# Kernel optimization log

Measured on AMD Instinct MI355X. Metric: run time of the kernel, lower is better.

The kernel has to match this reference:

```python
import jax, jax.numpy as jnp
import numpy as np

N_NODES = 100000
N_EDGES = 3200000
IN_FEATS = 512
HIDDEN = 16
NUM_CLASSES = 40


def setup_inputs() -> dict:
    key = jax.random.key(0)
    k1, k2, k3, k4, k5, k6 = jax.random.split(key, 6)
    x = jax.random.normal(k1, (N_NODES, IN_FEATS), dtype=jnp.float32)
    edge_index = jax.random.randint(k2, (2, N_EDGES), 0, N_NODES, dtype=jnp.int64)
    # Glorot-ish init for GCN weights
    W1 = jax.random.normal(k3, (IN_FEATS, HIDDEN), dtype=jnp.float32) / np.sqrt(IN_FEATS)
    b1 = jnp.zeros((HIDDEN,), dtype=jnp.float32)
    W2 = jax.random.normal(k4, (HIDDEN, NUM_CLASSES), dtype=jnp.float32) / np.sqrt(HIDDEN)
    b2 = jnp.zeros((NUM_CLASSES,), dtype=jnp.float32)
    return {"x": x, "edge_index": edge_index, "W1": W1, "b1": b1, "W2": W2, "b2": b2}


def _gcn_norm(edge_index, num_nodes):
    # Add self-loops (PyG GCNConv default), then symmetric normalization
    loops = jnp.arange(num_nodes, dtype=edge_index.dtype)
    src = jnp.concatenate([edge_index[0], loops])
    dst = jnp.concatenate([edge_index[1], loops])
    deg = jax.ops.segment_sum(jnp.ones_like(dst, dtype=jnp.float32), dst,
                              num_segments=num_nodes)
    dinv = jnp.where(deg > 0, jax.lax.rsqrt(deg), 0.0)
    norm = dinv[src] * dinv[dst]  # [E + N]
    return src, dst, norm


def _gcn_conv(x, W, b, src, dst, norm, num_nodes):
    h = x @ W                                   # transform first: [N, d_out]
    msg = h[src] * norm[:, None]                # gather + scale: [E+N, d_out]
    agg = jax.ops.segment_sum(msg, dst, num_segments=num_nodes)
    return agg + b


def reference(x, edge_index, W1, b1, W2, b2):
    num_nodes = x.shape[0]
    src, dst, norm = _gcn_norm(edge_index, num_nodes)
    h = _gcn_conv(x, W1, b1, src, dst, norm, num_nodes)
    h = jax.nn.relu(h)
    # F.dropout(training=self.training): eval mode -> identity (deterministic reference)
    h = _gcn_conv(h, W2, b2, src, dst, norm, num_nodes)
    return jax.nn.log_softmax(h, axis=1)
```

## Files before the change

### kernel.cpp

```cpp
#include <hip/hip_runtime.h>
#include <hip/hip_bf16.h>
#include <math.h>

#define N_NODES 100000
#define N_EDGES 3200000
#define IN_F    512
#define HID     16
#define NCLS    40
#define NB      2048
#define NPB     49
#define CAPW    2048
#define NBLK    256
#define EPB     12500
#define GEMM_BLKS 391

typedef unsigned short ushort_t;

__device__ __forceinline__ float bf16_to_f32(ushort_t u) {
    unsigned int b = ((unsigned int)u) << 16;
    return __uint_as_float(b);
}
__device__ __forceinline__ ushort_t f32_to_bf16(float f) {
    __hip_bfloat16 h = __float2bfloat16(f);
    return *(ushort_t*)&h;
}

__device__ __forceinline__ int load_edge(const void* ei, int is64, int idx) {
    if (is64) return (int)((const long long*)ei)[idx];
    return ((const int*)ei)[idx];
}

__global__ __launch_bounds__(256) void kPre(const int* __restrict__ ei,
                                            int* __restrict__ flag,
                                            int* __restrict__ gcur) {
    int i = blockIdx.x * 256 + threadIdx.x;
    if (i < NB) gcur[i] = i * CAPW;
    if (blockIdx.x == 0) {
        __shared__ int s_nz;
        if (threadIdx.x == 0) s_nz = 0;
        __syncthreads();
        int nz = 0;
        for (int k = threadIdx.x; k < 1024; k += 256)
            if (ei[2 * k + 1] != 0) nz = 1;
        if (nz) atomicOr(&s_nz, 1);
        __syncthreads();
        if (threadIdx.x == 0) flag[0] = s_nz ? 0 : 1;
    }
}

__global__ __launch_bounds__(256) void kMega(const float* __restrict__ x,
                                             const float* __restrict__ W1,
                                             ushort_t* __restrict__ hsb,
                                             const void* __restrict__ ei,
                                             const int* __restrict__ flag,
                                             int* __restrict__ gcur,
                                             int* __restrict__ binned) {
    __shared__ __align__(16) char smraw[IN_F * HID * 4];
    int tid = threadIdx.x;
    if (blockIdx.x < GEMM_BLKS) {
        float* Ws = (float*)smraw;
        for (int i = tid; i < IN_F * HID; i += 256) Ws[i] = W1[i];
        __syncthreads();
        int n = blockIdx.x * 256 + tid;
        if (n >= N_NODES) return;
        float acc[HID];
#pragma unroll
        for (int j = 0; j < HID; ++j) acc[j] = 0.0f;
        const float4* xr = (const float4*)(x + (size_t)n * IN_F);
        for (int k4 = 0; k4 < IN_F / 4; ++k4) {
            float4 xv = xr[k4];
            int kb = k4 * 4;
#pragma unroll
            for (int i = 0; i < 4; ++i) {
                float xs = (&xv.x)[i];
                const float4* wr = (const float4*)(Ws + (kb + i) * HID);
#pragma unroll
                for (int j4 = 0; j4 < 4; ++j4) {
                    float4 w = wr[j4];
                    acc[j4 * 4 + 0] += xs * w.x;
                    acc[j4 * 4 + 1] += xs * w.y;
                    acc[j4 * 4 + 2] += xs * w.z;
                    acc[j4 * 4 + 3] += xs * w.w;
                }
            }
        }
        ushort_t* hn = hsb + (size_t)n * HID;
#pragma unroll
        for (int j = 0; j < HID; ++j) hn[j] = f32_to_bf16(acc[j]);
    } else {
        int* hist = (int*)smraw;
        int* base = (int*)(smraw + NB * 4);
        for (int i = tid; i < NB; i += 256) hist[i] = 0;
        __syncthreads();
        int is64 = flag[0];
        int off0 = (blockIdx.x - GEMM_BLKS) * EPB;
        for (int i = tid; i < EPB; i += 256) {
            int d = load_edge(ei, is64, N_EDGES + off0 + i);
            atomicAdd(&hist[d / NPB], 1);
        }
        __syncthreads();
        for (int i = tid; i < NB; i += 256) {
            int c = hist[i];
            base[i] = c ? atomicAdd(&gcur[i], c) : 0;
            hist[i] = 0;
        }
        __syncthreads();
        for (int i = tid; i < EPB; i += 256) {
            int s = load_edge(ei, is64, off0 + i);
            int d = load_edge(ei, is64, N_EDGES + off0 + i);
            int b = d / NPB;
            int o = atomicAdd(&hist[b], 1);
            binned[base[b] + o] = (s << 6) | (d - b * NPB);
        }
    }
}

__global__ __launch_bounds__(256) void kSort(const int* __restrict__ gcur,
                                             int* __restrict__ binned,
                                             int* __restrict__ nstart,
                                             int* __restrict__ bend,
                                             float* __restrict__ dinv,
                                             ushort_t* __restrict__ hsb) {
    __shared__ int elist[CAPW];
    __shared__ int ih[NPB];
    __shared__ int lscan[NPB + 1];
    __shared__ float sdinv[NPB];
    int b = blockIdx.x, tid = threadIdx.x;
    int beg = b * CAPW;
    int cnt = gcur[b] - beg;
    if (cnt > CAPW) cnt = CAPW;
    if (cnt < 0) cnt = 0;
    if (tid < NPB) ih[tid] = 0;
    __syncthreads();
    for (int k = tid; k < cnt; k += 256) {
        int p = binned[beg + k];
        elist[k] = p;
        atomicAdd(&ih[p & 63], 1);
    }
    __syncthreads();
    if (tid == 0) {
        int run = 0;
        for (int i = 0; i < NPB; ++i) { lscan[i] = run; run += ih[i]; }
        lscan[NPB] = run;
        bend[b] = beg + run;
    }
    __syncthreads();
    if (tid < NPB) {
        int n = b * NPB + tid;
        float di = rsqrtf((float)(ih[tid] + 1));
        sdinv[tid] = di;
        if (n < N_NODES) dinv[n] = di;
        nstart[n] = beg + lscan[tid];
        ih[tid] = lscan[tid];
    }
    __syncthreads();
    for (int k = tid; k < cnt; k += 256) {
        int p = elist[k];
        int pos = atomicAdd(&ih[p & 63], 1);
        binned[beg + pos] = p >> 6;
    }
    for (int u = tid; u < NPB * HID; u += 256) {
        int i = u >> 4, j = u & 15;
        int n = b * NPB + i;
        if (n < N_NODES) {
            size_t idx = (size_t)n * HID + j;
            hsb[idx] = f32_to_bf16(bf16_to_f32(hsb[idx]) * sdinv[i]);
        }
    }
}

__global__ __launch_bounds__(256) void kAgg1(const int* __restrict__ nstart,
                                             const int* __restrict__ bend,
                                             const int* __restrict__ sorted,
                                             const ushort_t* __restrict__ hsb,
                                             const float* __restrict__ dinv,
                                             const float* __restrict__ b1,
                                             ushort_t* __restrict__ h1sb) {
    int tid = threadIdx.x;
    int g = tid >> 4, lane = tid & 15;
    int n = blockIdx.x * 16 + g;
    int b = n / NPB, il = n - b * NPB;
    int beg = nstart[n];
    int end = (il == NPB - 1) ? bend[b] : nstart[n + 1];
    float acc = 0.0f;
    int k = beg;
    for (; k + 4 <= end; k += 4) {
        int s0 = sorted[k + 0], s1 = sorted[k + 1];
        int s2 = sorted[k + 2], s3 = sorted[k + 3];
        float v0 = bf16_to_f32(hsb[(size_t)s0 * HID + lane]);
        float v1 = bf16_to_f32(hsb[(size_t)s1 * HID + lane]);
        float v2 = bf16_to_f32(hsb[(size_t)s2 * HID + lane]);
        float v3 = bf16_to_f32(hsb[(size_t)s3 * HID + lane]);
        acc += (v0 + v1) + (v2 + v3);
    }
    for (; k < end; ++k)
        acc += bf16_to_f32(hsb[(size_t)sorted[k] * HID + lane]);
    float di = dinv[n];
    float self = bf16_to_f32(hsb[(size_t)n * HID + lane]);
    float v = di * (acc + self) + b1[lane];
    h1sb[(size_t)n * HID + lane] = f32_to_bf16(fmaxf(v, 0.0f) * di);
}

__global__ __launch_bounds__(256) void kAggOut(const int* __restrict__ nstart,
                                               const int* __restrict__ bend,
                                               const int* __restrict__ sorted,
                                               const ushort_t* __restrict__ h1sb,
                                               const float* __restrict__ dinv,
                                               const float* __restrict__ W2,
                                               const float* __restrict__ b2,
                                               float* __restrict__ out) {
    __shared__ float a2[16][HID + 1];
    __shared__ float Ws[HID * NCLS];
    __shared__ float bs[NCLS];
    int tid = threadIdx.x;
    for (int i = tid; i < HID * NCLS; i += 256) Ws[i] = W2[i];
    for (int i = tid; i < NCLS; i += 256) bs[i] = b2[i];

    int g = tid >> 4, lane = tid & 15;
    int n = blockIdx.x * 16 + g;
    int b = n / NPB, il = n - b * NPB;
    int beg = nstart[n];
    int end = (il == NPB - 1) ? bend[b] : nstart[n + 1];
    float acc = 0.0f;
    int k = beg;
    for (; k + 4 <= end; k += 4) {
        int s0 = sorted[k + 0], s1 = sorted[k + 1];
        int s2 = sorted[k + 2], s3 = sorted[k + 3];
        float v0 = bf16_to_f32(h1sb[(size_t)s0 * HID + lane]);
        float v1 = bf16_to_f32(h1sb[(size_t)s1 * HID + lane]);
        float v2 = bf16_to_f32(h1sb[(size_t)s2 * HID + lane]);
        float v3 = bf16_to_f32(h1sb[(size_t)s3 * HID + lane]);
        acc += (v0 + v1) + (v2 + v3);
    }
    for (; k < end; ++k)
        acc += bf16_to_f32(h1sb[(size_t)sorted[k] * HID + lane]);
    float di = dinv[n];
    float self = bf16_to_f32(h1sb[(size_t)n * HID + lane]);
    a2[g][lane] = di * (acc + self);
    __syncthreads();

    int v = g, cidx = lane;
    float av[HID];
#pragma unroll
    for (int j = 0; j < HID; ++j) av[j] = a2[v][j];
    float l0 = bs[cidx], l1 = bs[cidx + 16];
    float l2 = (cidx < 8) ? bs[cidx + 32] : -1e30f;
#pragma unroll
    for (int j = 0; j < HID; ++j) {
        const float* wr = Ws + j * NCLS;
        l0 += av[j] * wr[cidx];
        l1 += av[j] * wr[cidx + 16];
        if (cidx < 8) l2 += av[j] * wr[cidx + 32];
    }
    float m = fmaxf(l0, fmaxf(l1, l2));
#pragma unroll
    for (int off = 8; off >= 1; off >>= 1)
        m = fmaxf(m, __shfl_xor(m, off, 16));
    float e = expf(l0 - m) + expf(l1 - m) + ((cidx < 8) ? expf(l2 - m) : 0.0f);
#pragma unroll
    for (int off = 8; off >= 1; off >>= 1)
        e += __shfl_xor(e, off, 16);
    float lse = m + logf(e);
    int nn = blockIdx.x * 16 + v;
    float* on = out + (size_t)nn * NCLS;
    on[cidx] = l0 - lse;
    on[cidx + 16] = l1 - lse;
    if (cidx < 8) on[cidx + 32] = l2 - lse;
}

extern "C" void kernel_launch(void* const* d_in, const int* in_sizes, int n_in,
                              void* d_out, int out_size, void* d_ws, size_t ws_size,
                              hipStream_t stream) {
    const float* x  = (const float*)d_in[0];
    const void*  ei = d_in[1];
    const float* W1 = (const float*)d_in[2];
    const float* b1 = (const float*)d_in[3];
    const float* W2 = (const float*)d_in[4];
    const float* b2 = (const float*)d_in[5];
    float* out = (float*)d_out;

    int*      iws    = (int*)d_ws;
    float*    fws    = (float*)d_ws;
    int*      gcur   = iws;
    int*      bend   = iws + 2048;
    int*      flag   = iws + 4096;
    float*    dinv   = fws + 8192;
    int*      nstart = iws + 108192;
    ushort_t* hsb    = (ushort_t*)(iws + 212992);
    ushort_t* h1sb   = (ushort_t*)(iws + 1012992);
    int*      binned = iws + 1812992;

    const int B = 256;

    kPre<<<(NB + B - 1) / B, B, 0, stream>>>((const int*)ei, flag, gcur);
    kMega<<<GEMM_BLKS + NBLK, B, 0, stream>>>(x, W1, hsb, ei, flag, gcur, binned);
    kSort<<<NB, B, 0, stream>>>(gcur, binned, nstart, bend, dinv, hsb);
    kAgg1<<<N_NODES / 16, B, 0, stream>>>(nstart, bend, binned, hsb, dinv, b1, h1sb);
    kAggOut<<<N_NODES / 16, B, 0, stream>>>(nstart, bend, binned, h1sb, dinv, W2, b2, out);
}
```

Baseline: 241.3 us.

## Coarsen destination buckets, add binning blocks, read W1 directly in GEMM

Cuts the destination buckets from 2048 to 512, so each bucket covers 196 nodes and holds up to 8192 entries. The local node index now takes 8 bits instead of 6. The binning phase uses 1024 blocks with fewer edges each, to spread the global histogram and scatter work. The fused GEMM part stops staging W1 in 32KB of shared memory and reads it from global/cache, which shrinks the kernel's LDS footprint and should raise occupancy. The trade-offs are fewer, heavier sort blocks with a longer serial prefix scan, and redundant global reads of W1.

```diff
diff --git a/kernel.cpp b/kernel.cpp
--- a/kernel.cpp
+++ b/kernel.cpp
@@ -7,12 +7,12 @@
 #define IN_F    512
 #define HID     16
 #define NCLS    40
-#define NB      2048
-#define NPB     49
-#define CAPW    2048
-#define NBLK    256
-#define EPB     12500
-#define GEMM_BLKS 391
+#define NB      512
+#define NPB     196
+#define CAPW    8192
+#define BBLK    1024
+#define EPB     3125
+#define GBLK    391
 
 typedef unsigned short ushort_t;
 
@@ -48,19 +48,17 @@
     }
 }
 
-__global__ __launch_bounds__(256) void kMega(const float* __restrict__ x,
-                                             const float* __restrict__ W1,
-                                             ushort_t* __restrict__ hsb,
-                                             const void* __restrict__ ei,
-                                             const int* __restrict__ flag,
-                                             int* __restrict__ gcur,
-                                             int* __restrict__ binned) {
-    __shared__ __align__(16) char smraw[IN_F * HID * 4];
+__global__ __launch_bounds__(256) void kMega2(const float* __restrict__ x,
+                                              const float* __restrict__ W1,
+                                              ushort_t* __restrict__ hsb,
+                                              const void* __restrict__ ei,
+                                              const int* __restrict__ flag,
+                                              int* __restrict__ gcur,
+                                              int* __restrict__ binned) {
+    __shared__ int hist[NB];
+    __shared__ int base[NB];
     int tid = threadIdx.x;
-    if (blockIdx.x < GEMM_BLKS) {
-        float* Ws = (float*)smraw;
-        for (int i = tid; i < IN_F * HID; i += 256) Ws[i] = W1[i];
-        __syncthreads();
+    if (blockIdx.x < GBLK) {
         int n = blockIdx.x * 256 + tid;
         if (n >= N_NODES) return;
         float acc[HID];
@@ -73,27 +71,19 @@
 #pragma unroll
             for (int i = 0; i < 4; ++i) {
                 float xs = (&xv.x)[i];
-                const float4* wr = (const float4*)(Ws + (kb + i) * HID);
-#pragma unroll
-                for (int j4 = 0; j4 < 4; ++j4) {
-                    float4 w = wr[j4];
-                    acc[j4 * 4 + 0] += xs * w.x;
-                    acc[j4 * 4 + 1] += xs * w.y;
-                    acc[j4 * 4 + 2] += xs * w.z;
-                    acc[j4 * 4 + 3] += xs * w.w;
-                }
+                const float* wr = W1 + (kb + i) * HID;
+#pragma unroll
+                for (int j = 0; j < HID; ++j) acc[j] += xs * wr[j];
             }
         }
         ushort_t* hn = hsb + (size_t)n * HID;
 #pragma unroll
         for (int j = 0; j < HID; ++j) hn[j] = f32_to_bf16(acc[j]);
     } else {
-        int* hist = (int*)smraw;
-        int* base = (int*)(smraw + NB * 4);
         for (int i = tid; i < NB; i += 256) hist[i] = 0;
         __syncthreads();
         int is64 = flag[0];
-        int off0 = (blockIdx.x - GEMM_BLKS) * EPB;
+        int off0 = (blockIdx.x - GBLK) * EPB;
         for (int i = tid; i < EPB; i += 256) {
             int d = load_edge(ei, is64, N_EDGES + off0 + i);
             atomicAdd(&hist[d / NPB], 1);
@@ -110,7 +100,7 @@
             int d = load_edge(ei, is64, N_EDGES + off0 + i);
             int b = d / NPB;
             int o = atomicAdd(&hist[b], 1);
-            binned[base[b] + o] = (s << 6) | (d - b * NPB);
+            binned[base[b] + o] = (s << 8) | (d - b * NPB);
         }
     }
 }
@@ -135,7 +125,7 @@
     for (int k = tid; k < cnt; k += 256) {
         int p = binned[beg + k];
         elist[k] = p;
-        atomicAdd(&ih[p & 63], 1);
+        atomicAdd(&ih[p & 255], 1);
     }
     __syncthreads();
     if (tid == 0) {
@@ -156,14 +146,14 @@
     __syncthreads();
     for (int k = tid; k < cnt; k += 256) {
         int p = elist[k];
-        int pos = atomicAdd(&ih[p & 63], 1);
-        binned[beg + pos] = p >> 6;
+        int pos = atomicAdd(&ih[p & 255], 1);
+        binned[beg + pos] = p >> 8;
     }
     for (int u = tid; u < NPB * HID; u += 256) {
-        int i = u >> 4, j = u & 15;
+        int i = u >> 4;
         int n = b * NPB + i;
         if (n < N_NODES) {
-            size_t idx = (size_t)n * HID + j;
+            size_t idx = (size_t)n * HID + (u & 15);
             hsb[idx] = f32_to_bf16(bf16_to_f32(hsb[idx]) * sdinv[i]);
         }
     }
@@ -239,33 +229,29 @@
     a2[g][lane] = di * (acc + self);
     __syncthreads();
 
-    int v = g, cidx = lane;
-    float av[HID];
-#pragma unroll
-    for (int j = 0; j < HID; ++j) av[j] = a2[v][j];
-    float l0 = bs[cidx], l1 = bs[cidx + 16];
-    float l2 = (cidx < 8) ? bs[cidx + 32] : -1e30f;
+    float l0 = bs[lane], l1 = bs[lane + 16];
+    float l2 = (lane < 8) ? bs[lane + 32] : -1e30f;
 #pragma unroll
     for (int j = 0; j < HID; ++j) {
+        float av = a2[g][j];
         const float* wr = Ws + j * NCLS;
-        l0 += av[j] * wr[cidx];
-        l1 += av[j] * wr[cidx + 16];
-        if (cidx < 8) l2 += av[j] * wr[cidx + 32];
+        l0 += av * wr[lane];
+        l1 += av * wr[lane + 16];
+        if (lane < 8) l2 += av * wr[lane + 32];
     }
     float m = fmaxf(l0, fmaxf(l1, l2));
 #pragma unroll
     for (int off = 8; off >= 1; off >>= 1)
         m = fmaxf(m, __shfl_xor(m, off, 16));
-    float e = expf(l0 - m) + expf(l1 - m) + ((cidx < 8) ? expf(l2 - m) : 0.0f);
+    float e = expf(l0 - m) + expf(l1 - m) + ((lane < 8) ? expf(l2 - m) : 0.0f);
 #pragma unroll
     for (int off = 8; off >= 1; off >>= 1)
         e += __shfl_xor(e, off, 16);
     float lse = m + logf(e);
-    int nn = blockIdx.x * 16 + v;
-    float* on = out + (size_t)nn * NCLS;
-    on[cidx] = l0 - lse;
-    on[cidx + 16] = l1 - lse;
-    if (cidx < 8) on[cidx + 32] = l2 - lse;
+    float* on = out + (size_t)n * NCLS;
+    on[lane] = l0 - lse;
+    on[lane + 16] = l1 - lse;
+    if (lane < 8) on[lane + 32] = l2 - lse;
 }
 
 extern "C" void kernel_launch(void* const* d_in, const int* in_sizes, int n_in,
@@ -293,7 +279,7 @@
     const int B = 256;
 
     kPre<<<(NB + B - 1) / B, B, 0, stream>>>((const int*)ei, flag, gcur);
-    kMega<<<GEMM_BLKS + NBLK, B, 0, stream>>>(x, W1, hsb, ei, flag, gcur, binned);
+    kMega2<<<GBLK + BBLK, B, 0, stream>>>(x, W1, hsb, ei, flag, gcur, binned);
     kSort<<<NB, B, 0, stream>>>(gcur, binned, nstart, bend, dinv, hsb);
     kAgg1<<<N_NODES / 16, B, 0, stream>>>(nstart, bend, binned, hsb, dinv, b1, h1sb);
     kAggOut<<<N_NODES / 16, B, 0, stream>>>(nstart, bend, binned, h1sb, dinv, W2, b2, out);
```

New measurement: 248.6 us. 1.03x slower.
